# Performance work log

Measured on AMD Instinct MI355X. Metric: run time of the kernel, lower is better.

## Reference

```python
import jax, jax.numpy as jnp
import numpy as np

B, T, K = 256, 64, 512


def setup_inputs() -> dict:
    key = jax.random.key(0)
    k1, k2, k3, k4, k5 = jax.random.split(key, 5)
    return {
        "x": jax.random.uniform(k1, (B, T), dtype=jnp.float32),          # soft binary evidence
        "prior_w": jax.random.normal(k2, (K,), dtype=jnp.float32),
        "emission_w": jax.random.normal(k3, (K, 2), dtype=jnp.float32),
        "coeff": jax.random.normal(k4, (K, K), dtype=jnp.float32),
        "bias": jax.random.normal(k5, (K, K), dtype=jnp.float32),
    }


def reference(x, prior_w, emission_w, coeff, bias):
    # emission: per-row softmax of [K,2] raw weights (TF loops rows; equivalent to axis=1 softmax)
    emission = jax.nn.softmax(emission_w, axis=1)  # [K, 2]

    def evidence(h, xt):
        # h: [B,K] (or broadcastable [1,K]); xt: [B]
        aug = jnp.stack([1.0 - xt, xt], axis=1)          # [B, 2]
        e = aug @ emission.T                             # [B, K]
        p = h * e                                        # [B, K]
        return p / jnp.sum(p, axis=1, keepdims=True)     # row-normalize (get_normalized_pr)

    prior = jax.nn.softmax(prior_w)                      # [K]
    post0 = evidence(prior[None, :], x[:, 0])            # [B, K]

    def step(post, xt):
        # transition_raw[i,j,k] = post[i,j]*coeff[j,k] + bias[j,k]
        raw = post[:, :, None] * coeff[None, :, :] + bias[None, :, :]   # [B, K, K]
        trans = jax.nn.softmax(raw, axis=2)              # get_normalized_pr_with_batch
        pbe = jnp.einsum('ij,ijk->ik', post, trans)      # [B, K]
        return evidence(pbe, xt), None

    post, _ = jax.lax.scan(step, post0, x[:, 1:].T)      # scan over time steps 1..T-1
    return post
```

## Files before the change

### kernel.cpp

```cpp
#include <hip/hip_runtime.h>

#define KDIM 512
#define TDIM 64
#define BDIM 256
#define NWAVE 16
#define BLOCK 1024
#define LOG2E 1.4426950408889634f

__device__ __forceinline__ float fast_exp2(float v) { return __builtin_amdgcn_exp2f(v); }
__device__ __forceinline__ float fast_rcp(float v)  { return __builtin_amdgcn_rcpf(v); }

__global__ __launch_bounds__(256) void prefold_kernel(
    const float* __restrict__ bias, float* __restrict__ b2)
{
    const int i = blockIdx.x * 256 + threadIdx.x;
    const float4 b = ((const float4*)bias)[i];
    ((float4*)b2)[i] = make_float4(b.x * LOG2E, b.y * LOG2E, b.z * LOG2E, b.w * LOG2E);
}

__device__ __forceinline__ float wave_reduce_sum(float v) {
    #pragma unroll
    for (int off = 1; off < 64; off <<= 1)
        v += __shfl_xor(v, off, 64);
    return v;
}

template <bool FOLDED>
__global__ __launch_bounds__(BLOCK)
__attribute__((amdgpu_waves_per_eu(4, 4)))
void hmm_forward_kernel(
    const float* __restrict__ x,
    const float* __restrict__ prior_w,
    const float* __restrict__ emission_w,
    const float* __restrict__ coeff,
    const float* __restrict__ bb,
    float* __restrict__ out)
{
    __shared__ float post[KDIM];
    __shared__ float em0s[KDIM];
    __shared__ float emds[KDIM];
    __shared__ float part[NWAVE][KDIM];
    __shared__ float rtmp[NWAVE];
    __shared__ float xs[TDIM];

    const int b    = blockIdx.x;
    const int tid  = threadIdx.x;
    const int lane = tid & 63;
    const int wv   = tid >> 6;
    const int k0   = 4 * lane;

    if (tid < TDIM) xs[tid] = x[b * TDIM + tid];
    if (tid < KDIM) {
        const float w0 = emission_w[2 * tid + 0];
        const float w1 = emission_w[2 * tid + 1];
        const float e0 = 1.0f / (1.0f + fast_exp2((w1 - w0) * LOG2E));
        em0s[tid] = e0;
        emds[tid] = 1.0f - 2.0f * e0;
    }
    __syncthreads();

    {
        const float x0 = xs[0];
        float v = 0.0f;
        if (tid < KDIM) {
            const float pr = fast_exp2(prior_w[tid] * LOG2E);
            v = pr * fmaf(x0, emds[tid], em0s[tid]);
        }
        float s = wave_reduce_sum(v);
        if (lane == 0) rtmp[wv] = s;
        __syncthreads();
        if (wv == 0) {
            float t2 = (lane < NWAVE) ? rtmp[lane] : 0.0f;
            #pragma unroll
            for (int off = 1; off < NWAVE; off <<= 1)
                t2 += __shfl_xor(t2, off, 64);
            if (lane == 0) rtmp[0] = t2;
        }
        __syncthreads();
        const float rn = fast_rcp(rtmp[0]);
        if (tid < KDIM) post[tid] = v * rn;
        __syncthreads();
    }

    for (int t = 1; t < TDIM; ++t) {
        float acc[8];
        #pragma unroll
        for (int i = 0; i < 8; ++i) acc[i] = 0.0f;

        const float* cA = coeff + (size_t)wv * KDIM + k0;
        const float* bA = bb    + (size_t)wv * KDIM + k0;
        const float* cB = cA + 16 * KDIM;
        const float* bB = bA + 16 * KDIM;

        #pragma unroll 1
        for (int i = 0; i < 16; ++i) {
            const float4 cA0 = *(const float4*)cA;
            const float4 cA1 = *(const float4*)(cA + 256);
            const float4 cB0 = *(const float4*)cB;
            const float4 cB1 = *(const float4*)(cB + 256);
            const float4 bA0 = *(const float4*)bA;
            const float4 bA1 = *(const float4*)(bA + 256);
            const float4 bB0 = *(const float4*)bB;
            const float4 bB1 = *(const float4*)(bB + 256);
            cA += 32 * KDIM; cB += 32 * KDIM;
            bA += 32 * KDIM; bB += 32 * KDIM;

            const float pA = post[wv + 32 * i];
            const float pB = post[wv + 16 + 32 * i];
            const float pAL = pA * LOG2E;
            const float pBL = pB * LOG2E;

            float eA0, eA1, eA2, eA3, eA4, eA5, eA6, eA7;
            float eB0, eB1, eB2, eB3, eB4, eB5, eB6, eB7;
            if (FOLDED) {
                eA0 = fast_exp2(fmaf(pAL, cA0.x, bA0.x));
                eA1 = fast_exp2(fmaf(pAL, cA0.y, bA0.y));
                eA2 = fast_exp2(fmaf(pAL, cA0.z, bA0.z));
                eA3 = fast_exp2(fmaf(pAL, cA0.w, bA0.w));
                eA4 = fast_exp2(fmaf(pAL, cA1.x, bA1.x));
                eA5 = fast_exp2(fmaf(pAL, cA1.y, bA1.y));
                eA6 = fast_exp2(fmaf(pAL, cA1.z, bA1.z));
                eA7 = fast_exp2(fmaf(pAL, cA1.w, bA1.w));
                eB0 = fast_exp2(fmaf(pBL, cB0.x, bB0.x));
                eB1 = fast_exp2(fmaf(pBL, cB0.y, bB0.y));
                eB2 = fast_exp2(fmaf(pBL, cB0.z, bB0.z));
                eB3 = fast_exp2(fmaf(pBL, cB0.w, bB0.w));
                eB4 = fast_exp2(fmaf(pBL, cB1.x, bB1.x));
                eB5 = fast_exp2(fmaf(pBL, cB1.y, bB1.y));
                eB6 = fast_exp2(fmaf(pBL, cB1.z, bB1.z));
                eB7 = fast_exp2(fmaf(pBL, cB1.w, bB1.w));
            } else {
                eA0 = fast_exp2(fmaf(pA, cA0.x, bA0.x) * LOG2E);
                eA1 = fast_exp2(fmaf(pA, cA0.y, bA0.y) * LOG2E);
                eA2 = fast_exp2(fmaf(pA, cA0.z, bA0.z) * LOG2E);
                eA3 = fast_exp2(fmaf(pA, cA0.w, bA0.w) * LOG2E);
                eA4 = fast_exp2(fmaf(pA, cA1.x, bA1.x) * LOG2E);
                eA5 = fast_exp2(fmaf(pA, cA1.y, bA1.y) * LOG2E);
                eA6 = fast_exp2(fmaf(pA, cA1.z, bA1.z) * LOG2E);
                eA7 = fast_exp2(fmaf(pA, cA1.w, bA1.w) * LOG2E);
                eB0 = fast_exp2(fmaf(pB, cB0.x, bB0.x) * LOG2E);
                eB1 = fast_exp2(fmaf(pB, cB0.y, bB0.y) * LOG2E);
                eB2 = fast_exp2(fmaf(pB, cB0.z, bB0.z) * LOG2E);
                eB3 = fast_exp2(fmaf(pB, cB0.w, bB0.w) * LOG2E);
                eB4 = fast_exp2(fmaf(pB, cB1.x, bB1.x) * LOG2E);
                eB5 = fast_exp2(fmaf(pB, cB1.y, bB1.y) * LOG2E);
                eB6 = fast_exp2(fmaf(pB, cB1.z, bB1.z) * LOG2E);
                eB7 = fast_exp2(fmaf(pB, cB1.w, bB1.w) * LOG2E);
            }

            float sA = ((eA0 + eA1) + (eA2 + eA3)) + ((eA4 + eA5) + (eA6 + eA7));
            float sB = ((eB0 + eB1) + (eB2 + eB3)) + ((eB4 + eB5) + (eB6 + eB7));
            #pragma unroll
            for (int off = 1; off < 64; off <<= 1) {
                sA += __shfl_xor(sA, off, 64);
                sB += __shfl_xor(sB, off, 64);
            }
            const float scA = pA * fast_rcp(sA);
            const float scB = pB * fast_rcp(sB);

            acc[0] = fmaf(scA, eA0, acc[0]); acc[0] = fmaf(scB, eB0, acc[0]);
            acc[1] = fmaf(scA, eA1, acc[1]); acc[1] = fmaf(scB, eB1, acc[1]);
            acc[2] = fmaf(scA, eA2, acc[2]); acc[2] = fmaf(scB, eB2, acc[2]);
            acc[3] = fmaf(scA, eA3, acc[3]); acc[3] = fmaf(scB, eB3, acc[3]);
            acc[4] = fmaf(scA, eA4, acc[4]); acc[4] = fmaf(scB, eB4, acc[4]);
            acc[5] = fmaf(scA, eA5, acc[5]); acc[5] = fmaf(scB, eB5, acc[5]);
            acc[6] = fmaf(scA, eA6, acc[6]); acc[6] = fmaf(scB, eB6, acc[6]);
            acc[7] = fmaf(scA, eA7, acc[7]); acc[7] = fmaf(scB, eB7, acc[7]);
        }

        *(float4*)(&part[wv][k0])       = make_float4(acc[0], acc[1], acc[2], acc[3]);
        *(float4*)(&part[wv][256 + k0]) = make_float4(acc[4], acc[5], acc[6], acc[7]);
        __syncthreads();

        float v = 0.0f;
        if (tid < KDIM) {
            float pbe = 0.0f;
            #pragma unroll
            for (int w2 = 0; w2 < NWAVE; ++w2) pbe += part[w2][tid];
            v = pbe * fmaf(xs[t], emds[tid], em0s[tid]);
        }
        float s = wave_reduce_sum(v);
        if (lane == 0) rtmp[wv] = s;
        __syncthreads();
        if (wv == 0) {
            float t2 = (lane < NWAVE) ? rtmp[lane] : 0.0f;
            #pragma unroll
            for (int off = 1; off < NWAVE; off <<= 1)
                t2 += __shfl_xor(t2, off, 64);
            if (lane == 0) rtmp[0] = t2;
        }
        __syncthreads();
        const float rn = fast_rcp(rtmp[0]);
        if (tid < KDIM) post[tid] = v * rn;
        __syncthreads();
    }

    if (tid < KDIM) out[b * KDIM + tid] = post[tid];
}

extern "C" void kernel_launch(void* const* d_in, const int* in_sizes, int n_in,
                              void* d_out, int out_size, void* d_ws, size_t ws_size,
                              hipStream_t stream) {
    const float* x          = (const float*)d_in[0];
    const float* prior_w    = (const float*)d_in[1];
    const float* emission_w = (const float*)d_in[2];
    const float* coeff      = (const float*)d_in[3];
    const float* bias       = (const float*)d_in[4];
    float* out              = (float*)d_out;

    const size_t need = (size_t)KDIM * KDIM * sizeof(float);
    if (ws_size >= need) {
        float* b2 = (float*)d_ws;
        hipLaunchKernelGGL(prefold_kernel, dim3(KDIM * KDIM / 4 / 256), dim3(256),
                           0, stream, bias, b2);
        hipLaunchKernelGGL((hmm_forward_kernel<true>), dim3(BDIM), dim3(BLOCK),
                           0, stream, x, prior_w, emission_w, coeff, b2, out);
    } else {
        hipLaunchKernelGGL((hmm_forward_kernel<false>), dim3(BDIM), dim3(BLOCK),
                           0, stream, x, prior_w, emission_w, coeff, bias, out);
    }
}
```

Baseline: 1.199 ms.

## Split each wave into four 16-lane groups, each handling a full row

Each wave is now divided into four 16-lane groups. Each group processes a whole 512-wide transition row, with 32 columns per lane, so the softmax row-sum reduction needs only 4 shuffle steps instead of 6. Per-lane accumulators grow from 8 to 32, and a cross-group shuffle reduction runs before writing the partial sums. The change trades fewer shuffles per row for much higher register pressure and possibly lower occupancy.

```diff
diff --git a/kernel.cpp b/kernel.cpp
--- a/kernel.cpp
+++ b/kernel.cpp
@@ -47,7 +47,8 @@
     const int tid  = threadIdx.x;
     const int lane = tid & 63;
     const int wv   = tid >> 6;
-    const int k0   = 4 * lane;
+    const int g    = lane >> 4;
+    const int l4   = lane & 15;
 
     if (tid < TDIM) xs[tid] = x[b * TDIM + tid];
     if (tid < KDIM) {
@@ -83,93 +84,73 @@
     }
 
     for (int t = 1; t < TDIM; ++t) {
-        float acc[8];
+        float acc[8][4];
         #pragma unroll
-        for (int i = 0; i < 8; ++i) acc[i] = 0.0f;
-
-        const float* cA = coeff + (size_t)wv * KDIM + k0;
-        const float* bA = bb    + (size_t)wv * KDIM + k0;
-        const float* cB = cA + 16 * KDIM;
-        const float* bB = bA + 16 * KDIM;
+        for (int m = 0; m < 8; ++m)
+            #pragma unroll
+            for (int q = 0; q < 4; ++q) acc[m][q] = 0.0f;
 
         #pragma unroll 1
-        for (int i = 0; i < 16; ++i) {
-            const float4 cA0 = *(const float4*)cA;
-            const float4 cA1 = *(const float4*)(cA + 256);
-            const float4 cB0 = *(const float4*)cB;
-            const float4 cB1 = *(const float4*)(cB + 256);
-            const float4 bA0 = *(const float4*)bA;
-            const float4 bA1 = *(const float4*)(bA + 256);
-            const float4 bB0 = *(const float4*)bB;
-            const float4 bB1 = *(const float4*)(bB + 256);
-            cA += 32 * KDIM; cB += 32 * KDIM;
-            bA += 32 * KDIM; bB += 32 * KDIM;
-
-            const float pA = post[wv + 32 * i];
-            const float pB = post[wv + 16 + 32 * i];
-            const float pAL = pA * LOG2E;
-            const float pBL = pB * LOG2E;
-
-            float eA0, eA1, eA2, eA3, eA4, eA5, eA6, eA7;
-            float eB0, eB1, eB2, eB3, eB4, eB5, eB6, eB7;
-            if (FOLDED) {
-                eA0 = fast_exp2(fmaf(pAL, cA0.x, bA0.x));
-                eA1 = fast_exp2(fmaf(pAL, cA0.y, bA0.y));
-                eA2 = fast_exp2(fmaf(pAL, cA0.z, bA0.z));
-                eA3 = fast_exp2(fmaf(pAL, cA0.w, bA0.w));
-                eA4 = fast_exp2(fmaf(pAL, cA1.x, bA1.x));
-                eA5 = fast_exp2(fmaf(pAL, cA1.y, bA1.y));
-                eA6 = fast_exp2(fmaf(pAL, cA1.z, bA1.z));
-                eA7 = fast_exp2(fmaf(pAL, cA1.w, bA1.w));
-                eB0 = fast_exp2(fmaf(pBL, cB0.x, bB0.x));
-                eB1 = fast_exp2(fmaf(pBL, cB0.y, bB0.y));
-                eB2 = fast_exp2(fmaf(pBL, cB0.z, bB0.z));
-                eB3 = fast_exp2(fmaf(pBL, cB0.w, bB0.w));
-                eB4 = fast_exp2(fmaf(pBL, cB1.x, bB1.x));
-                eB5 = fast_exp2(fmaf(pBL, cB1.y, bB1.y));
-                eB6 = fast_exp2(fmaf(pBL, cB1.z, bB1.z));
-                eB7 = fast_exp2(fmaf(pBL, cB1.w, bB1.w));
-            } else {
-                eA0 = fast_exp2(fmaf(pA, cA0.x, bA0.x) * LOG2E);
-                eA1 = fast_exp2(fmaf(pA, cA0.y, bA0.y) * LOG2E);
-                eA2 = fast_exp2(fmaf(pA, cA0.z, bA0.z) * LOG2E);
-                eA3 = fast_exp2(fmaf(pA, cA0.w, bA0.w) * LOG2E);
-                eA4 = fast_exp2(fmaf(pA, cA1.x, bA1.x) * LOG2E);
-                eA5 = fast_exp2(fmaf(pA, cA1.y, bA1.y) * LOG2E);
-                eA6 = fast_exp2(fmaf(pA, cA1.z, bA1.z) * LOG2E);
-                eA7 = fast_exp2(fmaf(pA, cA1.w, bA1.w) * LOG2E);
-                eB0 = fast_exp2(fmaf(pB, cB0.x, bB0.x) * LOG2E);
-                eB1 = fast_exp2(fmaf(pB, cB0.y, bB0.y) * LOG2E);
-                eB2 = fast_exp2(fmaf(pB, cB0.z, bB0.z) * LOG2E);
-                eB3 = fast_exp2(fmaf(pB, cB0.w, bB0.w) * LOG2E);
-                eB4 = fast_exp2(fmaf(pB, cB1.x, bB1.x) * LOG2E);
-                eB5 = fast_exp2(fmaf(pB, cB1.y, bB1.y) * LOG2E);
-                eB6 = fast_exp2(fmaf(pB, cB1.z, bB1.z) * LOG2E);
-                eB7 = fast_exp2(fmaf(pB, cB1.w, bB1.w) * LOG2E);
+        for (int i = 0; i < 8; ++i) {
+            const int j = wv + NWAVE * (4 * i + g);
+            const float p  = post[j];
+            const float pL = FOLDED ? (p * LOG2E) : p;
+
+            const float* crow = coeff + (size_t)j * KDIM + 4 * l4;
+            const float* brow = bb    + (size_t)j * KDIM + 4 * l4;
+
+            float e[8][4];
+            float s8[8];
+            #pragma unroll
+            for (int m = 0; m < 8; ++m) {
+                const float4 c  = *(const float4*)(crow + 64 * m);
+                const float4 bq = *(const float4*)(brow + 64 * m);
+                if (FOLDED) {
+                    e[m][0] = fast_exp2(fmaf(pL, c.x, bq.x));
+                    e[m][1] = fast_exp2(fmaf(pL, c.y, bq.y));
+                    e[m][2] = fast_exp2(fmaf(pL, c.z, bq.z));
+                    e[m][3] = fast_exp2(fmaf(pL, c.w, bq.w));
+                } else {
+                    e[m][0] = fast_exp2(fmaf(pL, c.x, bq.x) * LOG2E);
+                    e[m][1] = fast_exp2(fmaf(pL, c.y, bq.y) * LOG2E);
+                    e[m][2] = fast_exp2(fmaf(pL, c.z, bq.z) * LOG2E);
+                    e[m][3] = fast_exp2(fmaf(pL, c.w, bq.w) * LOG2E);
+                }
+                s8[m] = (e[m][0] + e[m][1]) + (e[m][2] + e[m][3]);
             }
 
-            float sA = ((eA0 + eA1) + (eA2 + eA3)) + ((eA4 + eA5) + (eA6 + eA7));
-            float sB = ((eB0 + eB1) + (eB2 + eB3)) + ((eB4 + eB5) + (eB6 + eB7));
-            #pragma unroll
-            for (int off = 1; off < 64; off <<= 1) {
-                sA += __shfl_xor(sA, off, 64);
-                sB += __shfl_xor(sB, off, 64);
+            float s = ((s8[0] + s8[1]) + (s8[2] + s8[3]))
+                    + ((s8[4] + s8[5]) + (s8[6] + s8[7]));
+            #pragma unroll
+            for (int off = 1; off < 16; off <<= 1)
+                s += __shfl_xor(s, off, 64);
+
+            const float sc = p * fast_rcp(s);
+            #pragma unroll
+            for (int m = 0; m < 8; ++m) {
+                acc[m][0] = fmaf(sc, e[m][0], acc[m][0]);
+                acc[m][1] = fmaf(sc, e[m][1], acc[m][1]);
+                acc[m][2] = fmaf(sc, e[m][2], acc[m][2]);
+                acc[m][3] = fmaf(sc, e[m][3], acc[m][3]);
             }
-            const float scA = pA * fast_rcp(sA);
-            const float scB = pB * fast_rcp(sB);
-
-            acc[0] = fmaf(scA, eA0, acc[0]); acc[0] = fmaf(scB, eB0, acc[0]);
-            acc[1] = fmaf(scA, eA1, acc[1]); acc[1] = fmaf(scB, eB1, acc[1]);
-            acc[2] = fmaf(scA, eA2, acc[2]); acc[2] = fmaf(scB, eB2, acc[2]);
-            acc[3] = fmaf(scA, eA3, acc[3]); acc[3] = fmaf(scB, eB3, acc[3]);
-            acc[4] = fmaf(scA, eA4, acc[4]); acc[4] = fmaf(scB, eB4, acc[4]);
-            acc[5] = fmaf(scA, eA5, acc[5]); acc[5] = fmaf(scB, eB5, acc[5]);
-            acc[6] = fmaf(scA, eA6, acc[6]); acc[6] = fmaf(scB, eB6, acc[6]);
-            acc[7] = fmaf(scA, eA7, acc[7]); acc[7] = fmaf(scB, eB7, acc[7]);
-        }
-
-        *(float4*)(&part[wv][k0])       = make_float4(acc[0], acc[1], acc[2], acc[3]);
-        *(float4*)(&part[wv][256 + k0]) = make_float4(acc[4], acc[5], acc[6], acc[7]);
+        }
+
+        #pragma unroll
+        for (int m = 0; m < 8; ++m) {
+            #pragma unroll
+            for (int q = 0; q < 4; ++q) {
+                float v = acc[m][q];
+                v += __shfl_xor(v, 16, 64);
+                v += __shfl_xor(v, 32, 64);
+                acc[m][q] = v;
+            }
+        }
+        if (lane < 16) {
+            #pragma unroll
+            for (int m = 0; m < 8; ++m)
+                *(float4*)(&part[wv][4 * l4 + 64 * m]) =
+                    make_float4(acc[m][0], acc[m][1], acc[m][2], acc[m][3]);
+        }
         __syncthreads();
 
         float v = 0.0f;
```

After: 1.252 ms. +4.4%, slower.
